# Kernel optimization log

Hardware: AMD Instinct MI355X
Metric: run time of the kernel (lower is better)

## Reference

```python
import jax, jax.numpy as jnp
import numpy as np

IOU_THR = 0.0  # module calls batched NMS with iou_threshold=0.0


def setup_inputs() -> dict:
    key = jax.random.key(0)
    kx, kc, kr = jax.random.split(key, 3)
    return {
        "x": jax.random.normal(kx, (10,), jnp.float32),
        "c": jax.random.normal(kc, (4,), jnp.float32),   # learned param
        "r": jax.random.normal(kr, (10,), jnp.float32),  # learned param
    }


def _pairwise_iou(b):
    # b: [n,4] (x1,y1,x2,y2); torchvision-style IoU (area not clamped, inter clamped at 0)
    x1, y1, x2, y2 = b[:, 0], b[:, 1], b[:, 2], b[:, 3]
    area = (x2 - x1) * (y2 - y1)
    iw = jnp.maximum(jnp.minimum(x2[:, None], x2[None, :]) - jnp.maximum(x1[:, None], x1[None, :]), 0.0)
    ih = jnp.maximum(jnp.minimum(y2[:, None], y2[None, :]) - jnp.maximum(y1[:, None], y1[None, :]), 0.0)
    inter = iw * ih
    return inter / (area[:, None] + area[None, :] - inter)


def _nms(boxes, scores, thr):
    # returns (order, keep_mask_in_sorted_order), fixed shapes (jit-safe)
    n = boxes.shape[0]
    order = jnp.argsort(-scores)
    iou = _pairwise_iou(boxes[order])
    j = jnp.arange(n)

    def body(i, keep):
        sup = (iou[i] > thr) & keep[i] & (j > i)
        return keep & ~sup

    keep = jax.lax.fori_loop(0, n, body, jnp.ones((n,), bool))
    return order, keep


def reference(x, c, r):
    boxes = jnp.outer(x, c)                      # [10,4]
    scores = r * x                               # [10]
    # batched-NMS coordinate trick: idxs = arange -> each box in its own class
    max_coord = boxes.max()
    offsets = jnp.arange(boxes.shape[0], dtype=boxes.dtype) * (max_coord + 1.0)
    boxes_nms = boxes + offsets[:, None]
    order, keep = _nms(boxes_nms, scores, IOU_THR)
    # torch returns boxes[keep] (dynamic shape). With distinct class ids all boxes
    # survive; we return fixed-shape [10,4] in keep order, suppressed rows zeroed.
    return jnp.where(keep[:, None], boxes[order], 0.0)
```

## Files before the change

### kernel.cpp

```cpp
#include <hip/hip_runtime.h>
#include <math.h>

#define N 10
#define C 4
#define NPAIR 45

__global__ __launch_bounds__(64, 1)
void Model_78056735637556_kernel(const float* __restrict__ x,
                                 const float* __restrict__ c,
                                 const float* __restrict__ r,
                                 float* __restrict__ out) {
    __shared__ float s_boxes[N][C];
    __shared__ float s_scores[N];
    __shared__ int   s_order[N];
    __shared__ int   s_mask[N];
    __shared__ float s_off;

    const int t = threadIdx.x;

    if (t < N * C) {
        const int i = t >> 2, k = t & 3;
        s_boxes[i][k] = x[i] * c[k];
    }
    if (t < N) { s_scores[t] = r[t] * x[t]; s_mask[t] = 0; }
    __syncthreads();

    if (t < N) {
        const float s = s_scores[t];
        int rank = 0;
        #pragma unroll
        for (int j = 0; j < N; ++j) {
            const float sj = s_scores[j];
            rank += (sj > s) || ((sj == s) && (j < t));
        }
        s_order[rank] = t;
    }
    if (t == N) {
        float m = -INFINITY;
        #pragma unroll
        for (int ii = 0; ii < N; ++ii)
            #pragma unroll
            for (int kk = 0; kk < C; ++kk)
                m = fmaxf(m, s_boxes[ii][kk]);
        s_off = m + 1.0f;
    }
    __syncthreads();

    if (t < NPAIR) {
        int p = 0, j = 1, acc = 0;
        #pragma unroll
        for (int pp = 0; pp < N - 1; ++pp) {
            const int cnt = N - 1 - pp;
            const bool in = (t >= acc) && (t < acc + cnt);
            p = in ? pp : p;
            j = in ? (pp + 1 + (t - acc)) : j;
            acc += cnt;
        }

        const float off = s_off;
        const int op = s_order[p];
        const int oj = s_order[j];
        const float dp = (float)op * off;
        const float dj = (float)oj * off;

        const float p0 = s_boxes[op][0] + dp, p1 = s_boxes[op][1] + dp;
        const float p2 = s_boxes[op][2] + dp, p3 = s_boxes[op][3] + dp;
        const float q0 = s_boxes[oj][0] + dj, q1 = s_boxes[oj][1] + dj;
        const float q2 = s_boxes[oj][2] + dj, q3 = s_boxes[oj][3] + dj;

        const float ap = (p2 - p0) * (p3 - p1);
        const float aq = (q2 - q0) * (q3 - q1);

        const float iw = fmaxf(fminf(p2, q2) - fmaxf(p0, q0), 0.0f);
        const float ih = fmaxf(fminf(p3, q3) - fmaxf(p1, q1), 0.0f);
        const float inter = iw * ih;
        const float iou = inter / (ap + aq - inter);

        if (iou > 0.0f)
            atomicOr(&s_mask[p], 1 << j);
    }
    __syncthreads();

    const int m0 = s_mask[0], m1 = s_mask[1], m2 = s_mask[2], m3 = s_mask[3];
    const int m4 = s_mask[4], m5 = s_mask[5], m6 = s_mask[6], m7 = s_mask[7];
    const int m8 = s_mask[8];
    int keep = (1 << N) - 1;
    if (keep & (1 << 0)) keep &= ~m0;
    if (keep & (1 << 1)) keep &= ~m1;
    if (keep & (1 << 2)) keep &= ~m2;
    if (keep & (1 << 3)) keep &= ~m3;
    if (keep & (1 << 4)) keep &= ~m4;
    if (keep & (1 << 5)) keep &= ~m5;
    if (keep & (1 << 6)) keep &= ~m6;
    if (keep & (1 << 7)) keep &= ~m7;
    if (keep & (1 << 8)) keep &= ~m8;

    if (t < N * C) {
        const int i = t >> 2, k = t & 3;
        out[t] = ((keep >> i) & 1) ? s_boxes[s_order[i]][k] : 0.0f;
    }
}

extern "C" void kernel_launch(void* const* d_in, const int* in_sizes, int n_in,
                              void* d_out, int out_size, void* d_ws, size_t ws_size,
                              hipStream_t stream) {
    const float* x = (const float*)d_in[0];
    const float* c = (const float*)d_in[1];
    const float* r = (const float*)d_in[2];
    float* out = (float*)d_out;
    Model_78056735637556_kernel<<<1, 64, 0, stream>>>(x, c, r, out);
}
```

Before: 57.89 us.

## Replace shared-memory stages with per-thread register compute and wave ballot

```diff
diff --git a/kernel.cpp b/kernel.cpp
--- a/kernel.cpp
+++ b/kernel.cpp
@@ -10,63 +10,72 @@
                                  const float* __restrict__ c,
                                  const float* __restrict__ r,
                                  float* __restrict__ out) {
-    __shared__ float s_boxes[N][C];
-    __shared__ float s_scores[N];
-    __shared__ int   s_order[N];
-    __shared__ int   s_mask[N];
-    __shared__ float s_off;
-
     const int t = threadIdx.x;
 
-    if (t < N * C) {
-        const int i = t >> 2, k = t & 3;
-        s_boxes[i][k] = x[i] * c[k];
-    }
-    if (t < N) { s_scores[t] = r[t] * x[t]; s_mask[t] = 0; }
-    __syncthreads();
+    float xs[N], rs[N], cs[C];
+    #pragma unroll
+    for (int q = 0; q < N; ++q) xs[q] = x[q];
+    #pragma unroll
+    for (int q = 0; q < C; ++q) cs[q] = c[q];
+    #pragma unroll
+    for (int q = 0; q < N; ++q) rs[q] = r[q];
 
-    if (t < N) {
-        const float s = s_scores[t];
+    float ss[N];
+    #pragma unroll
+    for (int q = 0; q < N; ++q) ss[q] = rs[q] * xs[q];
+
+    float m = -INFINITY;
+    #pragma unroll
+    for (int iq = 0; iq < N; ++iq)
+        #pragma unroll
+        for (int kq = 0; kq < C; ++kq)
+            m = fmaxf(m, xs[iq] * cs[kq]);
+    const float off = m + 1.0f;
+
+    int rk[N];
+    #pragma unroll
+    for (int j = 0; j < N; ++j) {
         int rank = 0;
         #pragma unroll
-        for (int j = 0; j < N; ++j) {
-            const float sj = s_scores[j];
-            rank += (sj > s) || ((sj == s) && (j < t));
-        }
-        s_order[rank] = t;
+        for (int q = 0; q < N; ++q)
+            rank += (q < j) ? (ss[q] >= ss[j]) : (ss[q] > ss[j]);
+        rk[j] = rank;
     }
-    if (t == N) {
-        float m = -INFINITY;
+
+    int pp_ = 0, jj_ = 1;
+    {
+        int acc = 0;
         #pragma unroll
-        for (int ii = 0; ii < N; ++ii)
-            #pragma unroll
-            for (int kk = 0; kk < C; ++kk)
-                m = fmaxf(m, s_boxes[ii][kk]);
-        s_off = m + 1.0f;
-    }
-    __syncthreads();
-
-    if (t < NPAIR) {
-        int p = 0, j = 1, acc = 0;
-        #pragma unroll
-        for (int pp = 0; pp < N - 1; ++pp) {
-            const int cnt = N - 1 - pp;
+        for (int pq = 0; pq < N - 1; ++pq) {
+            const int cnt = N - 1 - pq;
             const bool in = (t >= acc) && (t < acc + cnt);
-            p = in ? pp : p;
-            j = in ? (pp + 1 + (t - acc)) : j;
+            pp_ = in ? pq : pp_;
+            jj_ = in ? (pq + 1 + (t - acc)) : jj_;
             acc += cnt;
         }
+    }
 
-        const float off = s_off;
-        const int op = s_order[p];
-        const int oj = s_order[j];
+    int op = 0, oj = 0;
+    float xop = 0.0f, xoj = 0.0f;
+    #pragma unroll
+    for (int q = 0; q < N; ++q) {
+        const bool isp = (rk[q] == pp_);
+        const bool isj = (rk[q] == jj_);
+        op  = isp ? q     : op;
+        xop = isp ? xs[q] : xop;
+        oj  = isj ? q     : oj;
+        xoj = isj ? xs[q] : xoj;
+    }
+
+    bool sup;
+    {
+        #pragma clang fp contract(off)
         const float dp = (float)op * off;
         const float dj = (float)oj * off;
-
-        const float p0 = s_boxes[op][0] + dp, p1 = s_boxes[op][1] + dp;
-        const float p2 = s_boxes[op][2] + dp, p3 = s_boxes[op][3] + dp;
-        const float q0 = s_boxes[oj][0] + dj, q1 = s_boxes[oj][1] + dj;
-        const float q2 = s_boxes[oj][2] + dj, q3 = s_boxes[oj][3] + dj;
+        const float p0 = xop * cs[0] + dp, p1 = xop * cs[1] + dp;
+        const float p2 = xop * cs[2] + dp, p3 = xop * cs[3] + dp;
+        const float q0 = xoj * cs[0] + dj, q1 = xoj * cs[1] + dj;
+        const float q2 = xoj * cs[2] + dj, q3 = xoj * cs[3] + dj;
 
         const float ap = (p2 - p0) * (p3 - p1);
         const float aq = (q2 - q0) * (q3 - q1);
@@ -76,28 +85,32 @@
         const float inter = iw * ih;
         const float iou = inter / (ap + aq - inter);
 
-        if (iou > 0.0f)
-            atomicOr(&s_mask[p], 1 << j);
+        sup = (t < NPAIR) && (iou > 0.0f);
     }
-    __syncthreads();
 
-    const int m0 = s_mask[0], m1 = s_mask[1], m2 = s_mask[2], m3 = s_mask[3];
-    const int m4 = s_mask[4], m5 = s_mask[5], m6 = s_mask[6], m7 = s_mask[7];
-    const int m8 = s_mask[8];
+    const unsigned long long bal = __ballot(sup);
+
     int keep = (1 << N) - 1;
-    if (keep & (1 << 0)) keep &= ~m0;
-    if (keep & (1 << 1)) keep &= ~m1;
-    if (keep & (1 << 2)) keep &= ~m2;
-    if (keep & (1 << 3)) keep &= ~m3;
-    if (keep & (1 << 4)) keep &= ~m4;
-    if (keep & (1 << 5)) keep &= ~m5;
-    if (keep & (1 << 6)) keep &= ~m6;
-    if (keep & (1 << 7)) keep &= ~m7;
-    if (keep & (1 << 8)) keep &= ~m8;
+    #define ROW(P_, S_, L_)                                              \
+        if (keep & (1 << (P_))) {                                        \
+            const int bits = (int)((bal >> (S_)) & ((1ull << (L_)) - 1)); \
+            keep &= ~(bits << ((P_) + 1));                               \
+        }
+    ROW(0,  0, 9) ROW(1,  9, 8) ROW(2, 17, 7) ROW(3, 24, 6) ROW(4, 30, 5)
+    ROW(5, 35, 4) ROW(6, 39, 3) ROW(7, 42, 2) ROW(8, 44, 1)
+    #undef ROW
 
     if (t < N * C) {
         const int i = t >> 2, k = t & 3;
-        out[t] = ((keep >> i) & 1) ? s_boxes[s_order[i]][k] : 0.0f;
+        float xoi = 0.0f;
+        #pragma unroll
+        for (int q = 0; q < N; ++q)
+            xoi = (rk[q] == i) ? xs[q] : xoi;
+        float ck = cs[0];
+        ck = (k == 1) ? cs[1] : ck;
+        ck = (k == 2) ? cs[2] : ck;
+        ck = (k == 3) ? cs[3] : ck;
+        out[t] = ((keep >> i) & 1) ? xoi * ck : 0.0f;
     }
 }
 
```

Result: faster. 56.70 us (-2.0%).
